# Optimization experiments

Measured on AMD Instinct MI355X. Metric: run time of the kernel, lower is better.

Reference implementation:

```python
import jax, jax.numpy as jnp
import numpy as np

NUM_HEADS = 4
NUM_GROUPS = 8
EPS = 1e-5


def setup_inputs() -> dict:
    key = jax.random.key(0)
    ks = jax.random.split(key, 4)
    b, c, h, w = 16, 512, 32, 32
    x = jax.random.normal(ks[0], (b, c, h, w), dtype=jnp.float32)
    gamma = jnp.ones((c,), dtype=jnp.float32)
    beta = jnp.zeros((c,), dtype=jnp.float32)
    # conv1d kernel-size-1 weights expressed as [out, in] matrices
    w_qkv = jax.random.normal(ks[1], (3 * c, c), dtype=jnp.float32) * (1.0 / np.sqrt(c))
    b_qkv = jnp.zeros((3 * c,), dtype=jnp.float32)
    w_proj = jax.random.normal(ks[2], (c, c), dtype=jnp.float32) * (1.0 / np.sqrt(c))
    b_proj = jnp.zeros((c,), dtype=jnp.float32)
    return {"x": x, "gamma": gamma, "beta": beta, "w_qkv": w_qkv,
            "b_qkv": b_qkv, "w_proj": w_proj, "b_proj": b_proj}


def group_norm(x, gamma, beta):
    # x: [b, c, h, w]; normalize per (group) over (c/g, h, w)
    b, c, h, w = x.shape
    xg = x.reshape(b, NUM_GROUPS, c // NUM_GROUPS, h, w)
    mean = xg.mean(axis=(2, 3, 4), keepdims=True)
    var = xg.var(axis=(2, 3, 4), keepdims=True)
    xn = ((xg - mean) * jax.lax.rsqrt(var + EPS)).reshape(b, c, h, w)
    return xn * gamma[None, :, None, None] + beta[None, :, None, None]


def reference(x, gamma, beta, w_qkv, b_qkv, w_proj, b_proj):
    b, c, h, w = x.shape
    L = h * w
    hd = c // NUM_HEADS  # head_dim
    x_in = x
    xn = group_norm(x, gamma, beta).reshape(b, c, L)
    # 1x1 conv == matmul over channel dim: [b, 3c, L]
    qkv = jnp.einsum('oc,bcl->bol', w_qkv, xn) + b_qkv[None, :, None]
    q, k, v = jnp.split(qkv, 3, axis=1)  # each [b, c, L]
    q = q.reshape(b, NUM_HEADS, hd, L)
    k = k.reshape(b, NUM_HEADS, hd, L)
    v = v.reshape(b, NUM_HEADS, hd, L)
    scale = hd ** (-0.5)
    attn = jnp.einsum('bhdl,bhdm->bhlm', q * scale, k)  # [b,h,L,L]
    attn = jax.nn.softmax(attn, axis=-1)
    out = jnp.einsum('bhlm,bhdm->bhdl', attn, v).reshape(b, c, L)
    out = jnp.einsum('oc,bcl->bol', w_proj, out) + b_proj[None, :, None]
    return x_in + out.reshape(b, c, h, w)
```

## Files before the change

kernel.cpp:

```cpp
#include <hip/hip_runtime.h>
#include <hip/hip_bf16.h>

typedef __hip_bfloat16 bf16;
typedef __attribute__((ext_vector_type(8))) short short8;
typedef __attribute__((ext_vector_type(4))) float f32x4;

__device__ __forceinline__ float b2f(bf16 v) { return __bfloat162float(v); }
__device__ __forceinline__ bf16  f2b(float v) { return __float2bfloat16(v); }

__global__ __launch_bounds__(256) void convert_w_kernel(
    const float* __restrict__ wq, const float* __restrict__ wp,
    bf16* __restrict__ wqb, bf16* __restrict__ wpb)
{
    int ch = blockIdx.x * 256 + threadIdx.x;
    float4 v;
    bf16* dst;
    if (ch < 196608) {
        v = ((const float4*)wq)[ch];
        dst = wqb + ch * 4;
    } else {
        int c2 = ch - 196608;
        v = ((const float4*)wp)[c2];
        dst = wpb + c2 * 4;
    }
    bf16 o[4] = {f2b(v.x), f2b(v.y), f2b(v.z), f2b(v.w)};
    *(uint2*)dst = *(const uint2*)o;
}

__global__ __launch_bounds__(256) void gn_stats_kernel(
    const float* __restrict__ x,
    const float* __restrict__ gamma,
    const float* __restrict__ beta,
    float* __restrict__ scaleB, float* __restrict__ shiftB)
{
    const int bg = blockIdx.x;
    const int b = bg >> 3, g = bg & 7;
    const size_t base = ((size_t)(b * 512 + g * 64)) << 10;
    const int t = threadIdx.x;

    float sum = 0.f, ssq = 0.f;
    const float4* x4 = (const float4*)(x + base);
    for (int i = t; i < 16384; i += 256) {
        float4 v = x4[i];
        sum += v.x + v.y + v.z + v.w;
        ssq += v.x * v.x + v.y * v.y + v.z * v.z + v.w * v.w;
    }
    #pragma unroll
    for (int off = 32; off > 0; off >>= 1) {
        sum += __shfl_down(sum, off);
        ssq += __shfl_down(ssq, off);
    }
    __shared__ float red[8];
    const int wid = t >> 6, lane = t & 63;
    if (lane == 0) { red[wid] = sum; red[4 + wid] = ssq; }
    __syncthreads();
    if (t == 0) {
        float s = red[0] + red[1] + red[2] + red[3];
        float q = red[4] + red[5] + red[6] + red[7];
        float mean = s * (1.f / 65536.f);
        float var  = q * (1.f / 65536.f) - mean * mean;
        red[0] = mean;
        red[1] = rsqrtf(var + 1e-5f);
    }
    __syncthreads();
    if (t < 64) {
        const float mean = red[0], rstd = red[1];
        int c = g * 64 + t;
        float sc = rstd * gamma[c];
        scaleB[b * 512 + c] = sc;
        shiftB[b * 512 + c] = beta[c] - mean * sc;
    }
}

__global__ __launch_bounds__(256) void gn_apply_t_kernel(
    const float* __restrict__ x,
    const float* __restrict__ scaleB,
    const float* __restrict__ shiftB,
    bf16* __restrict__ Xt)
{
    const int lt = blockIdx.x, ct = blockIdx.y, b = blockIdx.z;
    const int l0 = lt * 64, c0 = ct * 64;
    const int t = threadIdx.x;
    __shared__ float Ls[64][65];

    const float* xb = x + ((size_t)b * 512 + c0) * 1024 + l0;
    for (int i = t; i < 1024; i += 256) {
        int cc = i >> 4, lc = (i & 15) * 4;
        float4 v = *(const float4*)(xb + (size_t)cc * 1024 + lc);
        float sc = scaleB[b * 512 + c0 + cc];
        float sh = shiftB[b * 512 + c0 + cc];
        Ls[cc][lc]     = v.x * sc + sh;
        Ls[cc][lc + 1] = v.y * sc + sh;
        Ls[cc][lc + 2] = v.z * sc + sh;
        Ls[cc][lc + 3] = v.w * sc + sh;
    }
    __syncthreads();
    for (int i = t; i < 1024; i += 256) {
        int l = i >> 4, cc = (i & 15) * 4;
        bf16 o[4] = {f2b(Ls[cc][l]), f2b(Ls[cc + 1][l]),
                     f2b(Ls[cc + 2][l]), f2b(Ls[cc + 3][l])};
        *(uint2*)(Xt + ((size_t)b * 1024 + l0 + l) * 512 + c0 + cc) = *(const uint2*)o;
    }
}

__global__ __launch_bounds__(256) void mfma_qkv_kernel(
    const bf16* __restrict__ W,
    const bf16* __restrict__ Xt,
    const float* __restrict__ bias,
    bf16* __restrict__ Qt,
    bf16* __restrict__ Kt,
    bf16* __restrict__ Vb)
{
    const int n0 = blockIdx.x * 128;
    const int m0 = blockIdx.y * 128;
    const int b  = blockIdx.z;
    const int t  = threadIdx.x;
    const int w  = t >> 6, lane = t & 63;
    const int c  = lane & 15, quad = lane >> 4;
    const int w0 = w & 1, w1 = w >> 1;
    const int ak = quad * 8;

    __shared__ __align__(16) bf16 smem[17408];
    bf16* As = smem;
    bf16* Bs = smem + 5120;
    bf16* Cs = smem;

    const bf16* Ag = W + (size_t)m0 * 512;
    const bf16* Bg = Xt + ((size_t)b * 1024 + n0) * 512;

    const int srow = t >> 2, skc = (t & 3) * 8;

    short8 areg[2], breg[2];
    #pragma unroll
    for (int it = 0; it < 2; it++) {
        int row = srow + it * 64;
        areg[it] = *(const short8*)(Ag + (size_t)row * 512 + skc);
        breg[it] = *(const short8*)(Bg + (size_t)row * 512 + skc);
    }

    f32x4 acc[4][4];
    #pragma unroll
    for (int i = 0; i < 4; i++)
        #pragma unroll
        for (int j = 0; j < 4; j++)
            #pragma unroll
            for (int r = 0; r < 4; r++) acc[i][j][r] = 0.f;

    for (int k0 = 0; k0 < 512; k0 += 32) {
        __syncthreads();
        #pragma unroll
        for (int it = 0; it < 2; it++) {
            int row = srow + it * 64;
            *(short8*)&As[row * 40 + skc] = areg[it];
            *(short8*)&Bs[row * 40 + skc] = breg[it];
        }
        __syncthreads();
        {
            int k1 = (k0 + 32) & 511;
            #pragma unroll
            for (int it = 0; it < 2; it++) {
                int row = srow + it * 64;
                areg[it] = *(const short8*)(Ag + (size_t)row * 512 + k1 + skc);
                breg[it] = *(const short8*)(Bg + (size_t)row * 512 + k1 + skc);
            }
        }
        short8 af[4], bf[4];
        #pragma unroll
        for (int jm = 0; jm < 4; jm++)
            af[jm] = *(const short8*)&As[(w0 * 64 + jm * 16 + c) * 40 + ak];
        #pragma unroll
        for (int jn = 0; jn < 4; jn++)
            bf[jn] = *(const short8*)&Bs[(w1 * 64 + jn * 16 + c) * 40 + ak];
        #pragma unroll
        for (int jm = 0; jm < 4; jm++)
            #pragma unroll
            for (int jn = 0; jn < 4; jn++)
                acc[jm][jn] = __builtin_amdgcn_mfma_f32_16x16x32_bf16(
                    af[jm], bf[jn], acc[jm][jn], 0, 0, 0);
    }

    __syncthreads();
    const int cls = m0 >> 9;
    if (cls < 2) {
        #pragma unroll
        for (int jm = 0; jm < 4; jm++) {
            #pragma unroll
            for (int jn = 0; jn < 4; jn++) {
                bf16 o4[4];
                #pragma unroll
                for (int r = 0; r < 4; r++) {
                    int orow = w0 * 64 + jm * 16 + quad * 4 + r;
                    o4[r] = f2b(acc[jm][jn][r] + bias[m0 + orow]);
                }
                *(uint2*)&Cs[(size_t)(w1 * 64 + jn * 16 + c) * 136
                             + w0 * 64 + jm * 16 + quad * 4] = *(const uint2*)o4;
            }
        }
        __syncthreads();
        const int head = (m0 >> 7) & 3;
        bf16* Db = (cls == 0 ? Qt : Kt)
                   + (((size_t)(b * 4 + head)) * 1024 + n0) * 128;
        for (int i = t; i < 2048; i += 256) {
            int row = i >> 4, ch = (i & 15) * 8;
            *(short8*)(Db + (size_t)row * 128 + ch) = *(const short8*)&Cs[row * 136 + ch];
        }
    } else {
        #pragma unroll
        for (int jm = 0; jm < 4; jm++) {
            #pragma unroll
            for (int r = 0; r < 4; r++) {
                int orow = w0 * 64 + jm * 16 + quad * 4 + r;
                float bs = bias[m0 + orow];
                #pragma unroll
                for (int jn = 0; jn < 4; jn++)
                    Cs[orow * 136 + w1 * 64 + jn * 16 + c] = f2b(acc[jm][jn][r] + bs);
            }
        }
        __syncthreads();
        bf16* Cb = Vb + ((size_t)b * 512 + (m0 - 1024)) * 1024 + n0;
        for (int i = t; i < 2048; i += 256) {
            int row = i >> 4, ch = (i & 15) * 8;
            *(short8*)(Cb + (size_t)row * 1024 + ch) = *(const short8*)&Cs[row * 136 + ch];
        }
    }
}

#define HD 128
#define QT 128
#define MT 64
#define SM_SHIFT 6.0f

__global__ __launch_bounds__(512, 4) void attn_mfma_kernel(
    const bf16* __restrict__ Qt,
    const bf16* __restrict__ Kt,
    const bf16* __restrict__ Vb,
    bf16* __restrict__ out)
{
    const int bh = blockIdx.x;
    const int qt = blockIdx.y;
    const int b = bh >> 2, h = bh & 3;
    const int t = threadIdx.x;
    const int w = t >> 6, lane = t & 63;
    const int c = lane & 15, quad = lane >> 4;
    const int l0 = qt * QT;
    const int arow = w * 16 + c;
    const int ak   = quad * 8;

    __shared__ __align__(16) bf16 smem[27136];
    bf16* Ks = smem;
    bf16* Vs = smem + 8704;
    bf16* Ps = smem + 17920;

    const bf16* Qrow = Qt + (((size_t)(b * 4 + h)) * 1024 + l0 + arow) * 128;
    short8 aq[4];
    #pragma unroll
    for (int kt = 0; kt < 4; kt++)
        aq[kt] = *(const short8*)(Qrow + kt * 32 + ak);

    const bf16* Kb = Kt + (((size_t)(b * 4 + h)) * 1024) * 128;
    const bf16* Vg = Vb + ((size_t)(b * 512 + h * HD)) * 1024;

    short8 kreg[2], vreg[2];
    #pragma unroll
    for (int p = 0; p < 2; p++) {
        int i = t + p * 512;
        kreg[p] = *(const short8*)(Kb + (size_t)(i >> 4) * 128 + (i & 15) * 8);
        vreg[p] = *(const short8*)(Vg + (size_t)(i >> 3) * 1024 + (i & 7) * 8);
    }

    f32x4 acc_o[8];
    #pragma unroll
    for (int n = 0; n < 8; n++)
        #pragma unroll
        for (int r = 0; r < 4; r++) acc_o[n][r] = 0.f;

    float psum_acc[4] = {0.f, 0.f, 0.f, 0.f};
    const float scale = 0.08838834764831845f;

    for (int mt = 0; mt < 1024 / MT; mt++) {
        __syncthreads();

        #pragma unroll
        for (int p = 0; p < 2; p++) {
            int i = t + p * 512;
            *(short8*)&Ks[(i >> 4) * 136 + (i & 15) * 8] = kreg[p];
            *(short8*)&Vs[(i >> 3) * 72 + (i & 7) * 8]   = vreg[p];
        }
        __syncthreads();

        {
            int m0n = (mt < 15) ? (mt + 1) * MT : 0;
            #pragma unroll
            for (int p = 0; p < 2; p++) {
                int i = t + p * 512;
                kreg[p] = *(const short8*)(Kb + (size_t)(m0n + (i >> 4)) * 128 + (i & 15) * 8);
                vreg[p] = *(const short8*)(Vg + (size_t)(i >> 3) * 1024 + m0n + (i & 7) * 8);
            }
        }

        f32x4 accs[4];
        #pragma unroll
        for (int j = 0; j < 4; j++)
            #pragma unroll
            for (int r = 0; r < 4; r++) accs[j][r] = 0.f;
        #pragma unroll
        for (int kt = 0; kt < 4; kt++) {
            #pragma unroll
            for (int j = 0; j < 4; j++) {
                short8 bf = *(const short8*)&Ks[(j * 16 + c) * 136 + kt * 32 + ak];
                accs[j] = __builtin_amdgcn_mfma_f32_16x16x32_bf16(aq[kt], bf, accs[j], 0, 0, 0);
            }
        }

        #pragma unroll
        for (int j = 0; j < 4; j++)
            #pragma unroll
            for (int r = 0; r < 4; r++) {
                float p = __expf(accs[j][r] * scale - SM_SHIFT);
                psum_acc[r] += p;
                Ps[(w * 16 + quad * 4 + r) * 72 + j * 16 + c] = f2b(p);
            }

        #pragma unroll
        for (int kt = 0; kt < 2; kt++) {
            short8 a = *(const short8*)&Ps[arow * 72 + kt * 32 + ak];
            #pragma unroll
            for (int n = 0; n < 8; n++) {
                short8 bf = *(const short8*)&Vs[(n * 16 + c) * 72 + kt * 32 + ak];
                acc_o[n] = __builtin_amdgcn_mfma_f32_16x16x32_bf16(a, bf, acc_o[n], 0, 0, 0);
            }
        }
    }

    #pragma unroll
    for (int off = 1; off < 16; off <<= 1)
        #pragma unroll
        for (int r = 0; r < 4; r++)
            psum_acc[r] += __shfl_xor(psum_acc[r], off);

    __syncthreads();
    bf16* Os = smem;
    float inv[4];
    #pragma unroll
    for (int r = 0; r < 4; r++) inv[r] = 1.f / psum_acc[r];
    #pragma unroll
    for (int n = 0; n < 8; n++) {
        #pragma unroll
        for (int r = 0; r < 4; r++) {
            int l = w * 16 + quad * 4 + r;
            Os[l * 136 + n * 16 + c] = f2b(acc_o[n][r] * inv[r]);
        }
    }
    __syncthreads();
    bf16* Ob = out + ((size_t)b * 1024 + l0) * 512 + h * HD;
    for (int i = t; i < 2048; i += 512) {
        int row = i >> 4, ch = (i & 15) * 8;
        *(short8*)(Ob + (size_t)row * 512 + ch) = *(const short8*)&Os[row * 136 + ch];
    }
}

__global__ __launch_bounds__(256) void mfma_proj_kernel(
    const bf16* __restrict__ W,
    const bf16* __restrict__ Xt,
    const float* __restrict__ bias,
    const float* __restrict__ res,
    float* __restrict__ C)
{
    const int n0 = blockIdx.x * 128;
    const int m0 = blockIdx.y * 128;
    const int b  = blockIdx.z;
    const int t  = threadIdx.x;
    const int w  = t >> 6, lane = t & 63;
    const int c  = lane & 15, quad = lane >> 4;
    const int w0 = w & 1, w1 = w >> 1;
    const int ak = quad * 8;

    __shared__ __align__(16) bf16 smem[17408];
    bf16* As = smem;
    bf16* Bs = smem + 5120;
    bf16* Cs = smem;

    const bf16* Ag = W + (size_t)m0 * 512;
    const bf16* Bg = Xt + ((size_t)b * 1024 + n0) * 512;

    const int srow = t >> 2, skc = (t & 3) * 8;

    short8 areg[2], breg[2];
    #pragma unroll
    for (int it = 0; it < 2; it++) {
        int row = srow + it * 64;
        areg[it] = *(const short8*)(Ag + (size_t)row * 512 + skc);
        breg[it] = *(const short8*)(Bg + (size_t)row * 512 + skc);
    }

    f32x4 acc[4][4];
    #pragma unroll
    for (int i = 0; i < 4; i++)
        #pragma unroll
        for (int j = 0; j < 4; j++)
            #pragma unroll
            for (int r = 0; r < 4; r++) acc[i][j][r] = 0.f;

    for (int k0 = 0; k0 < 512; k0 += 32) {
        __syncthreads();
        #pragma unroll
        for (int it = 0; it < 2; it++) {
            int row = srow + it * 64;
            *(short8*)&As[row * 40 + skc] = areg[it];
            *(short8*)&Bs[row * 40 + skc] = breg[it];
        }
        __syncthreads();
        {
            int k1 = (k0 + 32) & 511;
            #pragma unroll
            for (int it = 0; it < 2; it++) {
                int row = srow + it * 64;
                areg[it] = *(const short8*)(Ag + (size_t)row * 512 + k1 + skc);
                breg[it] = *(const short8*)(Bg + (size_t)row * 512 + k1 + skc);
            }
        }
        short8 af[4], bf[4];
        #pragma unroll
        for (int jm = 0; jm < 4; jm++)
            af[jm] = *(const short8*)&As[(w0 * 64 + jm * 16 + c) * 40 + ak];
        #pragma unroll
        for (int jn = 0; jn < 4; jn++)
            bf[jn] = *(const short8*)&Bs[(w1 * 64 + jn * 16 + c) * 40 + ak];
        #pragma unroll
        for (int jm = 0; jm < 4; jm++)
            #pragma unroll
            for (int jn = 0; jn < 4; jn++)
                acc[jm][jn] = __builtin_amdgcn_mfma_f32_16x16x32_bf16(
                    af[jm], bf[jn], acc[jm][jn], 0, 0, 0);
    }

    __syncthreads();
    #pragma unroll
    for (int jm = 0; jm < 4; jm++) {
        #pragma unroll
        for (int r = 0; r < 4; r++) {
            int orow = w0 * 64 + jm * 16 + quad * 4 + r;
            float bs = bias[m0 + orow];
            #pragma unroll
            for (int jn = 0; jn < 4; jn++)
                Cs[orow * 136 + w1 * 64 + jn * 16 + c] = f2b(acc[jm][jn][r] + bs);
        }
    }
    __syncthreads();
    const float* Rb = res + ((size_t)b * 512 + m0) * 1024 + n0;
    float* Cb = C + ((size_t)b * 512 + m0) * 1024 + n0;
    for (int i = t; i < 4096; i += 256) {
        int row = i >> 5, ch = (i & 31) * 4;
        float4 rv = *(const float4*)(Rb + (size_t)row * 1024 + ch);
        float4 ov;
        ov.x = b2f(Cs[row * 136 + ch + 0]) + rv.x;
        ov.y = b2f(Cs[row * 136 + ch + 1]) + rv.y;
        ov.z = b2f(Cs[row * 136 + ch + 2]) + rv.z;
        ov.w = b2f(Cs[row * 136 + ch + 3]) + rv.w;
        *(float4*)(Cb + (size_t)row * 1024 + ch) = ov;
    }
}

extern "C" void kernel_launch(void* const* d_in, const int* in_sizes, int n_in,
                              void* d_out, int out_size, void* d_ws, size_t ws_size,
                              hipStream_t stream)
{
    const float* x      = (const float*)d_in[0];
    const float* gamma  = (const float*)d_in[1];
    const float* beta   = (const float*)d_in[2];
    const float* w_qkv  = (const float*)d_in[3];
    const float* b_qkv  = (const float*)d_in[4];
    const float* w_proj = (const float*)d_in[5];
    const float* b_proj = (const float*)d_in[6];
    float* out = (float*)d_out;

    char* ws = (char*)d_ws;
    float* scaleB = (float*)ws;
    float* shiftB = (float*)(ws + 32768);
    bf16*  wqb    = (bf16*)(ws + 65536);
    bf16*  wpb    = (bf16*)(ws + 65536 + 1572864);
    char*  big    = ws + 65536 + 2097152;
    bf16*  Xt     = (bf16*)(big);
    bf16*  Qt     = (bf16*)(big + (size_t)16777216);
    bf16*  Kt     = (bf16*)(big + (size_t)2 * 16777216);
    bf16*  Vb     = (bf16*)(big + (size_t)3 * 16777216);
    bf16*  attn_t = Xt;

    hipLaunchKernelGGL(convert_w_kernel, dim3(1024), dim3(256), 0, stream,
                       w_qkv, w_proj, wqb, wpb);
    hipLaunchKernelGGL(gn_stats_kernel, dim3(128), dim3(256), 0, stream,
                       x, gamma, beta, scaleB, shiftB);
    hipLaunchKernelGGL(gn_apply_t_kernel, dim3(16, 8, 16), dim3(256), 0, stream,
                       x, scaleB, shiftB, Xt);
    hipLaunchKernelGGL(mfma_qkv_kernel, dim3(8, 12, 16), dim3(256), 0, stream,
                       wqb, Xt, b_qkv, Qt, Kt, Vb);
    hipLaunchKernelGGL(attn_mfma_kernel, dim3(64, 8), dim3(512), 0, stream,
                       Qt, Kt, Vb, attn_t);
    hipLaunchKernelGGL(mfma_proj_kernel, dim3(8, 4, 16), dim3(256), 0, stream,
                       wpb, attn_t, b_proj, x, out);
}
```

Baseline: 253.9 us.

## Use 32x32 MFMA tiles in attention and split group-norm stats reduction

The attention kernel moves from 8 waves each computing 16 query rows with 16x16x32 MFMAs to 4 waves each computing 32 rows with 32x32x16 MFMAs. This halves the block size and changes the register layout for scores, outputs and row sums. The larger tiles are meant to cut LDS fragment reads per FLOP and raise MFMA efficiency, at the cost of more registers per wave and fewer waves per block. Separately, the group-norm statistics pass is split into a 512-block partial-sum kernel plus a small finalize kernel, to use more CUs for the reduction over x, which adds one extra launch.

```diff
diff --git a/kernel.cpp b/kernel.cpp
--- a/kernel.cpp
+++ b/kernel.cpp
@@ -4,6 +4,7 @@
 typedef __hip_bfloat16 bf16;
 typedef __attribute__((ext_vector_type(8))) short short8;
 typedef __attribute__((ext_vector_type(4))) float f32x4;
+typedef __attribute__((ext_vector_type(16))) float f32x16;
 
 __device__ __forceinline__ float b2f(bf16 v) { return __bfloat162float(v); }
 __device__ __forceinline__ bf16  f2b(float v) { return __float2bfloat16(v); }
@@ -27,20 +28,17 @@
     *(uint2*)dst = *(const uint2*)o;
 }
 
-__global__ __launch_bounds__(256) void gn_stats_kernel(
+__global__ __launch_bounds__(256) void gn_partial_kernel(
     const float* __restrict__ x,
-    const float* __restrict__ gamma,
-    const float* __restrict__ beta,
-    float* __restrict__ scaleB, float* __restrict__ shiftB)
-{
-    const int bg = blockIdx.x;
-    const int b = bg >> 3, g = bg & 7;
-    const size_t base = ((size_t)(b * 512 + g * 64)) << 10;
+    float* __restrict__ partS, float* __restrict__ partQ)
+{
+    const int bid = blockIdx.x;
+    const size_t base = (size_t)bid * 16384;
     const int t = threadIdx.x;
 
     float sum = 0.f, ssq = 0.f;
     const float4* x4 = (const float4*)(x + base);
-    for (int i = t; i < 16384; i += 256) {
+    for (int i = t; i < 4096; i += 256) {
         float4 v = x4[i];
         sum += v.x + v.y + v.z + v.w;
         ssq += v.x * v.x + v.y * v.y + v.z * v.z + v.w * v.w;
@@ -55,21 +53,28 @@
     if (lane == 0) { red[wid] = sum; red[4 + wid] = ssq; }
     __syncthreads();
     if (t == 0) {
-        float s = red[0] + red[1] + red[2] + red[3];
-        float q = red[4] + red[5] + red[6] + red[7];
-        float mean = s * (1.f / 65536.f);
-        float var  = q * (1.f / 65536.f) - mean * mean;
-        red[0] = mean;
-        red[1] = rsqrtf(var + 1e-5f);
-    }
-    __syncthreads();
-    if (t < 64) {
-        const float mean = red[0], rstd = red[1];
-        int c = g * 64 + t;
-        float sc = rstd * gamma[c];
-        scaleB[b * 512 + c] = sc;
-        shiftB[b * 512 + c] = beta[c] - mean * sc;
-    }
+        partS[bid] = red[0] + red[1] + red[2] + red[3];
+        partQ[bid] = red[4] + red[5] + red[6] + red[7];
+    }
+}
+
+__global__ __launch_bounds__(64) void gn_finalize_kernel(
+    const float* __restrict__ partS, const float* __restrict__ partQ,
+    const float* __restrict__ gamma, const float* __restrict__ beta,
+    float* __restrict__ scaleB, float* __restrict__ shiftB)
+{
+    const int bg = blockIdx.x;
+    const int b = bg >> 3, g = bg & 7;
+    const int t = threadIdx.x;
+    float s = partS[bg * 4] + partS[bg * 4 + 1] + partS[bg * 4 + 2] + partS[bg * 4 + 3];
+    float q = partQ[bg * 4] + partQ[bg * 4 + 1] + partQ[bg * 4 + 2] + partQ[bg * 4 + 3];
+    float mean = s * (1.f / 65536.f);
+    float var  = q * (1.f / 65536.f) - mean * mean;
+    float rstd = rsqrtf(var + 1e-5f);
+    int c = g * 64 + t;
+    float sc = rstd * gamma[c];
+    scaleB[b * 512 + c] = sc;
+    shiftB[b * 512 + c] = beta[c] - mean * sc;
 }
 
 __global__ __launch_bounds__(256) void gn_apply_t_kernel(
@@ -230,7 +235,7 @@
 #define MT 64
 #define SM_SHIFT 6.0f
 
-__global__ __launch_bounds__(512, 4) void attn_mfma_kernel(
+__global__ __launch_bounds__(256, 2) void attn_mfma_kernel(
     const bf16* __restrict__ Qt,
     const bf16* __restrict__ Kt,
     const bf16* __restrict__ Vb,
@@ -241,48 +246,51 @@
     const int b = bh >> 2, h = bh & 3;
     const int t = threadIdx.x;
     const int w = t >> 6, lane = t & 63;
-    const int c = lane & 15, quad = lane >> 4;
+    const int wrow = lane & 31;
+    const int blk  = lane >> 5;
     const int l0 = qt * QT;
-    const int arow = w * 16 + c;
-    const int ak   = quad * 8;
 
     __shared__ __align__(16) bf16 smem[27136];
     bf16* Ks = smem;
     bf16* Vs = smem + 8704;
     bf16* Ps = smem + 17920;
 
-    const bf16* Qrow = Qt + (((size_t)(b * 4 + h)) * 1024 + l0 + arow) * 128;
-    short8 aq[4];
-    #pragma unroll
-    for (int kt = 0; kt < 4; kt++)
-        aq[kt] = *(const short8*)(Qrow + kt * 32 + ak);
+    const int qrow = w * 32 + wrow;
+    const bf16* Qr = Qt + (((size_t)(b * 4 + h)) * 1024 + l0 + qrow) * 128;
+    short8 aq[8];
+    #pragma unroll
+    for (int kt = 0; kt < 8; kt++)
+        aq[kt] = *(const short8*)(Qr + kt * 16 + blk * 8);
 
     const bf16* Kb = Kt + (((size_t)(b * 4 + h)) * 1024) * 128;
     const bf16* Vg = Vb + ((size_t)(b * 512 + h * HD)) * 1024;
 
-    short8 kreg[2], vreg[2];
-    #pragma unroll
-    for (int p = 0; p < 2; p++) {
-        int i = t + p * 512;
+    short8 kreg[4], vreg[4];
+    #pragma unroll
+    for (int p = 0; p < 4; p++) {
+        int i = t + p * 256;
         kreg[p] = *(const short8*)(Kb + (size_t)(i >> 4) * 128 + (i & 15) * 8);
         vreg[p] = *(const short8*)(Vg + (size_t)(i >> 3) * 1024 + (i & 7) * 8);
     }
 
-    f32x4 acc_o[8];
-    #pragma unroll
-    for (int n = 0; n < 8; n++)
-        #pragma unroll
-        for (int r = 0; r < 4; r++) acc_o[n][r] = 0.f;
-
-    float psum_acc[4] = {0.f, 0.f, 0.f, 0.f};
+    f32x16 acc_o[4];
+    #pragma unroll
+    for (int n = 0; n < 4; n++)
+        #pragma unroll
+        for (int r = 0; r < 16; r++) acc_o[n][r] = 0.f;
+
+    float psum[16];
+    #pragma unroll
+    for (int r = 0; r < 16; r++) psum[r] = 0.f;
+
     const float scale = 0.08838834764831845f;
 
     for (int mt = 0; mt < 1024 / MT; mt++) {
         __syncthreads();
 
         #pragma unroll
-        for (int p = 0; p < 2; p++) {
-            int i = t + p * 512;
+        for (int p = 0; p < 4; p++) {
+            int i = t + p * 256;
             *(short8*)&Ks[(i >> 4) * 136 + (i & 15) * 8] = kreg[p];
             *(short8*)&Vs[(i >> 3) * 72 + (i & 7) * 8]   = vreg[p];
         }
@@ -291,69 +299,69 @@
         {
             int m0n = (mt < 15) ? (mt + 1) * MT : 0;
             #pragma unroll
-            for (int p = 0; p < 2; p++) {
-                int i = t + p * 512;
+            for (int p = 0; p < 4; p++) {
+                int i = t + p * 256;
                 kreg[p] = *(const short8*)(Kb + (size_t)(m0n + (i >> 4)) * 128 + (i & 15) * 8);
                 vreg[p] = *(const short8*)(Vg + (size_t)(i >> 3) * 1024 + m0n + (i & 7) * 8);
             }
         }
 
-        f32x4 accs[4];
-        #pragma unroll
-        for (int j = 0; j < 4; j++)
-            #pragma unroll
-            for (int r = 0; r < 4; r++) accs[j][r] = 0.f;
-        #pragma unroll
-        for (int kt = 0; kt < 4; kt++) {
-            #pragma unroll
-            for (int j = 0; j < 4; j++) {
-                short8 bf = *(const short8*)&Ks[(j * 16 + c) * 136 + kt * 32 + ak];
-                accs[j] = __builtin_amdgcn_mfma_f32_16x16x32_bf16(aq[kt], bf, accs[j], 0, 0, 0);
-            }
-        }
-
-        #pragma unroll
-        for (int j = 0; j < 4; j++)
-            #pragma unroll
-            for (int r = 0; r < 4; r++) {
-                float p = __expf(accs[j][r] * scale - SM_SHIFT);
-                psum_acc[r] += p;
-                Ps[(w * 16 + quad * 4 + r) * 72 + j * 16 + c] = f2b(p);
-            }
-
-        #pragma unroll
-        for (int kt = 0; kt < 2; kt++) {
-            short8 a = *(const short8*)&Ps[arow * 72 + kt * 32 + ak];
-            #pragma unroll
-            for (int n = 0; n < 8; n++) {
-                short8 bf = *(const short8*)&Vs[(n * 16 + c) * 72 + kt * 32 + ak];
-                acc_o[n] = __builtin_amdgcn_mfma_f32_16x16x32_bf16(a, bf, acc_o[n], 0, 0, 0);
-            }
-        }
-    }
-
-    #pragma unroll
-    for (int off = 1; off < 16; off <<= 1)
-        #pragma unroll
-        for (int r = 0; r < 4; r++)
-            psum_acc[r] += __shfl_xor(psum_acc[r], off);
+        f32x16 accs[2];
+        #pragma unroll
+        for (int n = 0; n < 2; n++)
+            #pragma unroll
+            for (int r = 0; r < 16; r++) accs[n][r] = 0.f;
+        #pragma unroll
+        for (int kt = 0; kt < 8; kt++) {
+            #pragma unroll
+            for (int nt = 0; nt < 2; nt++) {
+                short8 bfr = *(const short8*)&Ks[(nt * 32 + wrow) * 136 + kt * 16 + blk * 8];
+                accs[nt] = __builtin_amdgcn_mfma_f32_32x32x16_bf16(aq[kt], bfr, accs[nt], 0, 0, 0);
+            }
+        }
+
+        #pragma unroll
+        for (int nt = 0; nt < 2; nt++)
+            #pragma unroll
+            for (int r = 0; r < 16; r++) {
+                float p = __expf(accs[nt][r] * scale - SM_SHIFT);
+                psum[r] += p;
+                int row = w * 32 + (r & 3) + 8 * (r >> 2) + 4 * blk;
+                Ps[row * 72 + nt * 32 + wrow] = f2b(p);
+            }
+
+        #pragma unroll
+        for (int kt2 = 0; kt2 < 4; kt2++) {
+            short8 a = *(const short8*)&Ps[(w * 32 + wrow) * 72 + kt2 * 16 + blk * 8];
+            #pragma unroll
+            for (int nt2 = 0; nt2 < 4; nt2++) {
+                short8 bv = *(const short8*)&Vs[(nt2 * 32 + wrow) * 72 + kt2 * 16 + blk * 8];
+                acc_o[nt2] = __builtin_amdgcn_mfma_f32_32x32x16_bf16(a, bv, acc_o[nt2], 0, 0, 0);
+            }
+        }
+    }
+
+    #pragma unroll
+    for (int off = 1; off < 32; off <<= 1)
+        #pragma unroll
+        for (int r = 0; r < 16; r++)
+            psum[r] += __shfl_xor(psum[r], off);
 
     __syncthreads();
     bf16* Os = smem;
-    float inv[4];
-    #pragma unroll
-    for (int r = 0; r < 4; r++) inv[r] = 1.f / psum_acc[r];
-    #pragma unroll
-    for (int n = 0; n < 8; n++) {
-        #pragma unroll
-        for (int r = 0; r < 4; r++) {
-            int l = w * 16 + quad * 4 + r;
-            Os[l * 136 + n * 16 + c] = f2b(acc_o[n][r] * inv[r]);
-        }
-    }
+    float inv[16];
+    #pragma unroll
+    for (int r = 0; r < 16; r++) inv[r] = 1.f / psum[r];
+    #pragma unroll
+    for (int nt2 = 0; nt2 < 4; nt2++)
+        #pragma unroll
+        for (int r = 0; r < 16; r++) {
+            int row = w * 32 + (r & 3) + 8 * (r >> 2) + 4 * blk;
+            Os[row * 136 + nt2 * 32 + wrow] = f2b(acc_o[nt2][r] * inv[r]);
+        }
     __syncthreads();
     bf16* Ob = out + ((size_t)b * 1024 + l0) * 512 + h * HD;
-    for (int i = t; i < 2048; i += 512) {
+    for (int i = t; i < 2048; i += 256) {
         int row = i >> 4, ch = (i & 15) * 8;
         *(short8*)(Ob + (size_t)row * 512 + ch) = *(const short8*)&Os[row * 136 + ch];
     }
@@ -484,17 +492,21 @@
     bf16*  Qt     = (bf16*)(big + (size_t)16777216);
     bf16*  Kt     = (bf16*)(big + (size_t)2 * 16777216);
     bf16*  Vb     = (bf16*)(big + (size_t)3 * 16777216);
+    float* partS  = (float*)(big + (size_t)4 * 16777216);
+    float* partQ  = partS + 512;
     bf16*  attn_t = Xt;
 
     hipLaunchKernelGGL(convert_w_kernel, dim3(1024), dim3(256), 0, stream,
                        w_qkv, w_proj, wqb, wpb);
-    hipLaunchKernelGGL(gn_stats_kernel, dim3(128), dim3(256), 0, stream,
-                       x, gamma, beta, scaleB, shiftB);
+    hipLaunchKernelGGL(gn_partial_kernel, dim3(512), dim3(256), 0, stream,
+                       x, partS, partQ);
+    hipLaunchKernelGGL(gn_finalize_kernel, dim3(128), dim3(64), 0, stream,
+                       partS, partQ, gamma, beta, scaleB, shiftB);
     hipLaunchKernelGGL(gn_apply_t_kernel, dim3(16, 8, 16), dim3(256), 0, stream,
                        x, scaleB, shiftB, Xt);
     hipLaunchKernelGGL(mfma_qkv_kernel, dim3(8, 12, 16), dim3(256), 0, stream,
                        wqb, Xt, b_qkv, Qt, Kt, Vb);
-    hipLaunchKernelGGL(attn_mfma_kernel, dim3(64, 8), dim3(512), 0, stream,
+    hipLaunchKernelGGL(attn_mfma_kernel, dim3(64, 8), dim3(256), 0, stream,
                        Qt, Kt, Vb, attn_t);
     hipLaunchKernelGGL(mfma_proj_kernel, dim3(8, 4, 16), dim3(256), 0, stream,
                        wpb, attn_t, b_proj, x, out);
```

Measured after the change: 228.0 us. 1.11x faster.
